# Kernel optimization log

Measured on AMD Instinct MI355X. Metric: run time of the kernel, lower is better.

Reference implementation:

```python
import jax, jax.numpy as jnp
import numpy as np

N = 100000   # nodes
E = 1600000  # edges
G = 64       # graphs in batch
DIMS = [(7, 128), (128, 128), (128, 256)]
EPS = 1e-5


def setup_inputs() -> dict:
    key = jax.random.key(0)
    ks = jax.random.split(key, 32)
    inp = {}
    inp["x"] = jax.random.normal(ks[0], (N, 7), dtype=jnp.float32)
    inp["edge_index"] = jax.random.randint(ks[1], (2, E), 0, N, dtype=jnp.int64)
    inp["batch"] = jnp.sort(jax.random.randint(ks[2], (N,), 0, G, dtype=jnp.int64))
    ki = 3
    for i, (din, dout) in enumerate(DIMS):
        inp[f"Wl{i}"] = jax.random.normal(ks[ki], (din, dout), dtype=jnp.float32) * 0.05; ki += 1
        inp[f"bl{i}"] = jnp.zeros((dout,), dtype=jnp.float32)
        inp[f"Wr{i}"] = jax.random.normal(ks[ki], (din, dout), dtype=jnp.float32) * 0.05; ki += 1
        inp[f"g{i}"] = jax.random.uniform(ks[ki], (dout,), dtype=jnp.float32) + 0.5; ki += 1
        inp[f"be{i}"] = jax.random.normal(ks[ki], (dout,), dtype=jnp.float32) * 0.1; ki += 1
        inp[f"rm{i}"] = jax.random.normal(ks[ki], (dout,), dtype=jnp.float32) * 0.1; ki += 1
        inp[f"rv{i}"] = jax.random.uniform(ks[ki], (dout,), dtype=jnp.float32) + 0.5; ki += 1
    return inp


def _sage(x, src, dst, Wl, bl, Wr):
    # mean-aggregate neighbor features: out[i] = mean_{(j->i)} x[j]
    agg = jax.ops.segment_sum(x[src], dst, num_segments=N)          # [N, din]
    cnt = jax.ops.segment_sum(jnp.ones((src.shape[0],), x.dtype), dst, num_segments=N)
    mean = agg / jnp.maximum(cnt, 1.0)[:, None]
    return x @ Wl + bl + mean @ Wr


def _bn_relu(x, g, be, rm, rv):
    # BatchNorm1d in eval mode (running stats) + ReLU; dropout is a no-op in eval
    return jax.nn.relu((x - rm) * jax.lax.rsqrt(rv + EPS) * g + be)


def reference(x, edge_index, batch,
              Wl0, bl0, Wr0, g0, be0, rm0, rv0,
              Wl1, bl1, Wr1, g1, be1, rm1, rv1,
              Wl2, bl2, Wr2, g2, be2, rm2, rv2):
    src, dst = edge_index[0], edge_index[1]
    layers = [(Wl0, bl0, Wr0, g0, be0, rm0, rv0),
              (Wl1, bl1, Wr1, g1, be1, rm1, rv1),
              (Wl2, bl2, Wr2, g2, be2, rm2, rv2)]
    for Wl, bl, Wr, g, be, rm, rv in layers:
        x = _sage(x, src, dst, Wl, bl, Wr)
        x = _bn_relu(x, g, be, rm, rv)
    pooled = jax.ops.segment_sum(x, batch, num_segments=G)  # global_add_pool
    return (pooled, x)
```

## Files before the change

### kernel.cpp

```cpp
#include <hip/hip_runtime.h>
#include <hip/hip_bf16.h>

#define EPSV 1e-5f
#define PSHIFT 6
#define PMASK 63
#define PCAP 1536
#define B1SHIFT 11
#define B1MASK ((1 << B1SHIFT) - 1)
#define B1CAP 34816
#define SPLIT 16

typedef __attribute__((ext_vector_type(8))) short bf16x8;
typedef __attribute__((ext_vector_type(4))) float f32x4;
typedef __attribute__((ext_vector_type(4))) unsigned u32x4;

__device__ __forceinline__ float bf2f(unsigned short u) {
    unsigned x = ((unsigned)u) << 16;
    return __builtin_bit_cast(float, x);
}
__device__ __forceinline__ unsigned short f2bf(float f) {
    unsigned x = __builtin_bit_cast(unsigned, f);
    unsigned r = (x + 0x7fffu + ((x >> 16) & 1u)) >> 16;
    return (unsigned short)r;
}
__device__ __forceinline__ f32x4 bflo4(u32x4 v) {
    f32x4 r;
    r.x = __builtin_bit_cast(float, v.x << 16);
    r.y = __builtin_bit_cast(float, v.y << 16);
    r.z = __builtin_bit_cast(float, v.z << 16);
    r.w = __builtin_bit_cast(float, v.w << 16);
    return r;
}
__device__ __forceinline__ f32x4 bfhi4(u32x4 v) {
    f32x4 r;
    r.x = __builtin_bit_cast(float, v.x & 0xffff0000u);
    r.y = __builtin_bit_cast(float, v.y & 0xffff0000u);
    r.z = __builtin_bit_cast(float, v.z & 0xffff0000u);
    r.w = __builtin_bit_cast(float, v.w & 0xffff0000u);
    return r;
}


__global__ __launch_bounds__(256) void k_scatter1(const int* __restrict__ src,
                                                  const int* __restrict__ dst,
                                                  int* __restrict__ bcnt1,
                                                  unsigned* __restrict__ stg1,
                                                  int E, int NB1) {
    __shared__ int hist[64], sbase[64], scur[64];
    int t = threadIdx.x;
    int base = blockIdx.x * 2048;
    if (t < 64) { hist[t] = 0; scur[t] = 0; }
    __syncthreads();
    unsigned val[8];
    int cb[8];
#pragma unroll
    for (int k = 0; k < 8; k++) {
        int i = base + k * 256 + t;
        if (i < E) {
            int d = __builtin_nontemporal_load(&dst[i]);
            int s = __builtin_nontemporal_load(&src[i]);
            cb[k] = d >> B1SHIFT;
            val[k] = ((unsigned)s << B1SHIFT) | (unsigned)(d & B1MASK);
            atomicAdd(&hist[cb[k]], 1);
        } else
            cb[k] = -1;
    }
    __syncthreads();
    if (t < NB1 && hist[t] > 0) sbase[t] = atomicAdd(&bcnt1[t], hist[t]);
    __syncthreads();
#pragma unroll
    for (int k = 0; k < 8; k++) {
        if (cb[k] >= 0) {
            int r = atomicAdd(&scur[cb[k]], 1);
            int slot = sbase[cb[k]] + r;
            if (slot < B1CAP) stg1[(size_t)cb[k] * B1CAP + slot] = val[k];
        }
    }
}

__global__ __launch_bounds__(256) void k_scatter2(const int* __restrict__ bcnt1,
                                                  const unsigned* __restrict__ stg1,
                                                  int* __restrict__ pcnt,
                                                  unsigned* __restrict__ pstg) {
    __shared__ int hist[32], sbase[32], scur[32];
    int cb = blockIdx.x >> 4;
    int sl = blockIdx.x & (SPLIT - 1);
    int t = threadIdx.x;
    if (t < 32) { hist[t] = 0; scur[t] = 0; }
    int cnt = min(bcnt1[cb], B1CAP);
    int per = (cnt + SPLIT - 1) / SPLIT;
    int lo = sl * per, hi = min(lo + per, cnt);
    __syncthreads();
    const unsigned* sp = stg1 + (size_t)cb * B1CAP;
    for (int j = lo + t; j < hi; j += 256)
        atomicAdd(&hist[(sp[j] >> 6) & 31], 1);
    __syncthreads();
    if (t < 32 && hist[t] > 0) sbase[t] = atomicAdd(&pcnt[(cb << 5) + t], hist[t]);
    __syncthreads();
    for (int j = lo + t; j < hi; j += 256) {
        unsigned v = sp[j];
        int pr = (v >> 6) & 31;
        int r = atomicAdd(&scur[pr], 1);
        int slot = sbase[pr] + r;
        if (slot < PCAP)
            pstg[(size_t)((cb << 5) + pr) * PCAP + slot] =
                ((v >> 5) & ~63u) | (v & 63u);
    }
}

__global__ __launch_bounds__(256) void k_meta(const int* __restrict__ pcnt,
                                              int* __restrict__ pbase,
                                              int* __restrict__ off,
                                              const int* __restrict__ batch,
                                              int* __restrict__ gstart,
                                              int NPART, int Nn, int G) {
    if (blockIdx.x == 1) {
        int g = threadIdx.x;
        if (g > G) return;
        if (g == G) {
            gstart[G] = Nn;
            return;
        }
        int lo = 0, hi = Nn;
        while (lo < hi) {
            int mid = (lo + hi) >> 1;
            if (batch[mid] < g) lo = mid + 1;
            else hi = mid;
        }
        gstart[g] = lo;
        return;
    }
    __shared__ int red[256];
    int t = threadIdx.x;
    int chunk = (NPART + 255) / 256;
    int lo = t * chunk, hi = min(lo + chunk, NPART);
    int s = 0;
    for (int p = lo; p < hi; p++) {
        int tt = min(pcnt[p], PCAP);
        pbase[p] = tt;
        s += tt;
    }
    red[t] = s;
    __syncthreads();
    for (int d = 1; d < 256; d <<= 1) {
        int v = (t >= d) ? red[t - d] : 0;
        __syncthreads();
        red[t] += v;
        __syncthreads();
    }
    int base = (t == 0) ? 0 : red[t - 1];
    for (int p = lo; p < hi; p++) {
        int tt = pbase[p];
        pbase[p] = base;
        base += tt;
    }
    if (t == 255) off[Nn] = red[255];
}

__global__ __launch_bounds__(256) void k_build(const int* __restrict__ pcnt,
                                               const unsigned* __restrict__ pstg,
                                               const int* __restrict__ pbase,
                                               int* __restrict__ off,
                                               int* __restrict__ csr, int Nn) {
    __shared__ unsigned ed[PCAP];
    __shared__ int srt[PCAP];
    __shared__ int cnt[64], loff[64], cur[64];
    int p = blockIdx.x, t = threadIdx.x;
    int tot = min(pcnt[p], PCAP);
    if (t < 64) cnt[t] = 0;
    __syncthreads();
    const unsigned* sp = pstg + (size_t)p * PCAP;
    for (int j = t; j < tot; j += 256) {
        unsigned e = __builtin_nontemporal_load(&sp[j]);
        ed[j] = e;
        atomicAdd(&cnt[e & PMASK], 1);
    }
    __syncthreads();
    if (t == 0) {
        int a = 0;
        for (int j = 0; j < 64; j++) {
            loff[j] = a;
            cur[j] = a;
            a += cnt[j];
        }
    }
    __syncthreads();
    int base = pbase[p];
    int node0 = p << PSHIFT;
    if (t < 64 && node0 + t < Nn) off[node0 + t] = base + loff[t];
    for (int j = t; j < tot; j += 256) {
        unsigned e = ed[j];
        int pos = atomicAdd(&cur[e & PMASK], 1);
        srt[pos] = (int)(e >> PSHIFT);
    }
    __syncthreads();
    for (int j = t; j < tot; j += 256) csr[base + j] = srt[j];
}


__global__ __launch_bounds__(256) void k_agg7(const float* __restrict__ x,
                                              const int* __restrict__ off,
                                              const int* __restrict__ csr,
                                              float* __restrict__ mean, int n) {
    int i = (blockIdx.x * 256 + threadIdx.x) >> 3;
    int r = threadIdx.x & 7;
    if (i >= n) return;
    int a = off[i], b = off[i + 1];
    float acc = 0.f;
    if (r < 7) {
        int j = a;
        for (; j + 1 < b; j += 2)
            acc += x[(size_t)csr[j] * 7 + r] + x[(size_t)csr[j + 1] * 7 + r];
        if (j < b) acc += x[(size_t)csr[j] * 7 + r];
    }
    float inv = 1.0f / (float)max(b - a, 1);
    if (r < 7) mean[(size_t)i * 7 + r] = acc * inv;
}

__global__ __launch_bounds__(256) void k_agg128(const unsigned short* __restrict__ x,
                                                const int* __restrict__ off,
                                                const int* __restrict__ csr,
                                                unsigned short* __restrict__ mean,
                                                int n) {
    int q = (blockIdx.x * 256 + threadIdx.x) >> 4;
    int sl = threadIdx.x & 15;
    if (q >= n) return;
    int a = off[q], b = off[q + 1];
    const u32x4* xr = (const u32x4*)x;
    f32x4 aL = {0.f, 0.f, 0.f, 0.f}, aH = {0.f, 0.f, 0.f, 0.f};
    int j = a;
    for (; j + 3 < b; j += 4) {
        int s0 = csr[j], s1 = csr[j + 1], s2 = csr[j + 2], s3 = csr[j + 3];
        u32x4 v0 = xr[(size_t)s0 * 16 + sl];
        u32x4 v1 = xr[(size_t)s1 * 16 + sl];
        u32x4 v2 = xr[(size_t)s2 * 16 + sl];
        u32x4 v3 = xr[(size_t)s3 * 16 + sl];
        aL += bflo4(v0) + bflo4(v1) + bflo4(v2) + bflo4(v3);
        aH += bfhi4(v0) + bfhi4(v1) + bfhi4(v2) + bfhi4(v3);
    }
    for (; j < b; j++) {
        u32x4 v = xr[(size_t)csr[j] * 16 + sl];
        aL += bflo4(v);
        aH += bfhi4(v);
    }
    float inv = 1.0f / (float)max(b - a, 1);
    u32x4 o;
    o.x = (unsigned)f2bf(aL.x * inv) | ((unsigned)f2bf(aH.x * inv) << 16);
    o.y = (unsigned)f2bf(aL.y * inv) | ((unsigned)f2bf(aH.y * inv) << 16);
    o.z = (unsigned)f2bf(aL.z * inv) | ((unsigned)f2bf(aH.z * inv) << 16);
    o.w = (unsigned)f2bf(aL.w * inv) | ((unsigned)f2bf(aH.w * inv) << 16);
    __builtin_nontemporal_store(o, (u32x4*)mean + (size_t)q * 16 + sl);
}


__global__ __launch_bounds__(256) void k_prepw_all(
    const float* __restrict__ Wl1, const float* __restrict__ Wr1,
    const float* __restrict__ Wl2, const float* __restrict__ Wr2,
    unsigned short* __restrict__ Wlt1, unsigned short* __restrict__ Wrt1,
    unsigned short* __restrict__ Wlt2, unsigned short* __restrict__ Wrt2) {
    int u = blockIdx.x * 256 + threadIdx.x;
    const float* W;
    unsigned short* Wt;
    int Ncols, v;
    if (u < 32768) {
        v = u & 16383;
        W = (u < 16384) ? Wl1 : Wr1;
        Wt = (u < 16384) ? Wlt1 : Wrt1;
        Ncols = 128;
    } else {
        v = (u - 32768) & 32767;
        W = (u < 65536) ? Wl2 : Wr2;
        Wt = (u < 65536) ? Wlt2 : Wrt2;
        Ncols = 256;
    }
    int n = v % Ncols, k = v / Ncols;
    Wt[(size_t)n * 128 + k] = f2bf(W[(size_t)k * Ncols + n]);
}


__global__ __launch_bounds__(256) void k_layer0(
    const float* __restrict__ x, const float* __restrict__ mean,
    const float* __restrict__ Wl, const float* __restrict__ bl,
    const float* __restrict__ Wr, const float* __restrict__ g,
    const float* __restrict__ be, const float* __restrict__ rm,
    const float* __restrict__ rv, unsigned short* __restrict__ out, int n) {
    int tid = threadIdx.x;
    int col = tid & 127;
    int r = tid >> 7;
    int row = blockIdx.x * 2 + r;
    if (row >= n) return;
    float sc = g[col] * rsqrtf(rv[col] + EPSV);
    float sh = (bl[col] - rm[col]) * sc + be[col];
    const float* xp = x + (size_t)row * 7;
    const float* mp = mean + (size_t)row * 7;
    float acc = 0.f;
#pragma unroll
    for (int k = 0; k < 7; k++) acc += xp[k] * Wl[k * 128 + col];
#pragma unroll
    for (int k = 0; k < 7; k++) acc += mp[k] * Wr[k * 128 + col];
    float h = acc * sc + sh;
    out[(size_t)row * 128 + col] = f2bf(fmaxf(h, 0.f));
}


template <int COLS, int DOUT, bool BF16OUT>
__global__ __launch_bounds__(256) void k_mfma_layer(
    const unsigned short* __restrict__ xin, const unsigned short* __restrict__ meanb,
    const unsigned short* __restrict__ Wlt, const unsigned short* __restrict__ Wrt,
    const float* __restrict__ bl, const float* __restrict__ g,
    const float* __restrict__ be, const float* __restrict__ rm,
    const float* __restrict__ rv, void* __restrict__ outv,
    const int* __restrict__ batchp, float* __restrict__ pooled, int n) {
    __shared__ unsigned short As[64 * 40];
    __shared__ unsigned short Bs[COLS * 40];
    __shared__ float plds[COLS];

    int tid = threadIdx.x;
    int wave = tid >> 6;
    int lane = tid & 63;
    int m = lane & 15;
    int half = lane >> 4;
    int row0 = blockIdx.x * 64;
    int colbase = blockIdx.y * COLS;

    if (!BF16OUT && tid < COLS) plds[tid] = 0.f;

    const int NCB = COLS / 16;
    f32x4 acc[NCB] = {};

    for (int s = 0; s < 8; s++) {
        int pass = s >> 2;
        int k0 = (s & 3) * 32;
        const unsigned short* Asrc = pass ? meanb : xin;
        const unsigned short* Wt = pass ? Wrt : Wlt;

        __syncthreads();
        {
            int rr = tid >> 2;
            int ks = (tid & 3) * 8;
            int grow = row0 + rr;
            float4 v = make_float4(0.f, 0.f, 0.f, 0.f);
            if (grow < n) v = *(const float4*)&Asrc[(size_t)grow * 128 + k0 + ks];
            *(float4*)&As[rr * 40 + ks] = v;
        }
#pragma unroll
        for (int rep = 0; rep < COLS / 64; rep++) {
            int u = tid + rep * 256;
            int nn = u >> 2;
            int ks = (u & 3) * 8;
            float4 v = *(const float4*)&Wt[(size_t)(colbase + nn) * 128 + k0 + ks];
            *(float4*)&Bs[nn * 40 + ks] = v;
        }
        __syncthreads();

        bf16x8 a = *(const bf16x8*)&As[(wave * 16 + m) * 40 + half * 8];
#pragma unroll
        for (int cb = 0; cb < NCB; cb++) {
            bf16x8 b = *(const bf16x8*)&Bs[(cb * 16 + m) * 40 + half * 8];
            acc[cb] = __builtin_amdgcn_mfma_f32_16x16x32_bf16(a, b, acc[cb], 0, 0, 0);
        }
    }

    bool uni = true;
    int gmin = 0;
    if (!BF16OUT) {
        int last = min(row0 + 63, n - 1);
        gmin = batchp[row0];
        uni = (gmin == batchp[last]);
    }

    float* outf = (float*)outv;
    unsigned short* outb = (unsigned short*)outv;
    float colsum[NCB];
#pragma unroll
    for (int cb = 0; cb < NCB; cb++) colsum[cb] = 0.f;

#pragma unroll
    for (int cb = 0; cb < NCB; cb++) {
        int col = colbase + cb * 16 + m;
        float sc = g[col] * rsqrtf(rv[col] + EPSV);
        float sh = (bl[col] - rm[col]) * sc + be[col];
#pragma unroll
        for (int reg = 0; reg < 4; reg++) {
            int r0 = row0 + wave * 16 + half * 4 + reg;
            if (r0 < n) {
                float h = fmaxf(acc[cb][reg] * sc + sh, 0.f);
                if (BF16OUT) {
                    outb[(size_t)r0 * DOUT + col] = f2bf(h);
                } else {
                    outf[(size_t)r0 * DOUT + col] = h;
                    if (uni) colsum[cb] += h;
                    else atomicAdd(&pooled[(size_t)batchp[r0] * 256 + col], h);
                }
            }
        }
    }

    if (!BF16OUT) {
        if (uni) {
#pragma unroll
            for (int cb = 0; cb < NCB; cb++) atomicAdd(&plds[cb * 16 + m], colsum[cb]);
            __syncthreads();
            if (tid < COLS)
                atomicAdd(&pooled[(size_t)gmin * 256 + colbase + tid], plds[tid]);
        }
    }
}


extern "C" void kernel_launch(void* const* d_in, const int* in_sizes, int n_in,
                              void* d_out, int out_size, void* d_ws, size_t ws_size,
                              hipStream_t stream) {
    const float* x = (const float*)d_in[0];
    const int* ei = (const int*)d_in[1];
    const int* batch = (const int*)d_in[2];
    const int N = in_sizes[0] / 7;
    const int E = in_sizes[1] / 2;
    const int G = 64;
    const int* src = ei;
    const int* dst = ei + E;
    const int NPART = (N + PMASK) >> PSHIFT;
    const int NB1 = (N + (1 << B1SHIFT) - 1) >> B1SHIFT;

    const float* P[21];
    for (int i = 0; i < 21; i++) P[i] = (const float*)d_in[3 + i];
    const float **L0 = P, **L1 = P + 7, **L2 = P + 14;

    char* w = (char*)d_ws;
    auto carve = [&](size_t bytes) {
        void* p = (void*)w;
        w += (bytes + 255) & ~(size_t)255;
        return p;
    };
    int* cnts = (int*)carve((size_t)(64 + NPART) * 4);
    int* bcnt1 = cnts;
    int* pcnt = cnts + 64;
    unsigned* stg1 = (unsigned*)carve((size_t)NB1 * B1CAP * 4);
    unsigned* pstg = (unsigned*)carve((size_t)NPART * PCAP * 4);
    int* pbase = (int*)carve((size_t)NPART * 4);
    int* off = (int*)carve(((size_t)N + 1) * 4);
    int* gstart = (int*)carve(((size_t)G + 1) * 4);
    float* mean7 = (float*)carve((size_t)N * 7 * 4);
    unsigned short* x1 = (unsigned short*)carve((size_t)N * 128 * 2);
    unsigned short* meanb = (unsigned short*)carve((size_t)N * 128 * 2);
    unsigned short* Wlt1 = (unsigned short*)carve((size_t)128 * 128 * 2);
    unsigned short* Wrt1 = (unsigned short*)carve((size_t)128 * 128 * 2);
    unsigned short* Wlt2 = (unsigned short*)carve((size_t)128 * 256 * 2);
    unsigned short* Wrt2 = (unsigned short*)carve((size_t)128 * 256 * 2);
    int* csr = (int*)stg1;

    float* pooled = (float*)d_out;
    float* x3 = (float*)d_out + (size_t)G * 256;

    hipMemsetAsync(cnts, 0, (size_t)(64 + NPART) * 4, stream);
    hipMemsetAsync(pooled, 0, (size_t)G * 256 * 4, stream);

    k_scatter1<<<(E + 2047) / 2048, 256, 0, stream>>>(src, dst, bcnt1, stg1, E, NB1);
    k_scatter2<<<NB1 * SPLIT, 256, 0, stream>>>(bcnt1, stg1, pcnt, pstg);
    k_meta<<<2, 256, 0, stream>>>(pcnt, pbase, off, batch, gstart, NPART, N, G);
    k_build<<<NPART, 256, 0, stream>>>(pcnt, pstg, pbase, off, csr, N);
    k_prepw_all<<<(98304 + 255) / 256, 256, 0, stream>>>(L1[0], L1[2], L2[0], L2[2],
                                                         Wlt1, Wrt1, Wlt2, Wrt2);

    k_agg7<<<(N * 8 + 255) / 256, 256, 0, stream>>>(x, off, csr, mean7, N);
    k_layer0<<<(N + 1) / 2, 256, 0, stream>>>(x, mean7, L0[0], L0[1], L0[2], L0[3],
                                              L0[4], L0[5], L0[6], x1, N);

    k_agg128<<<((size_t)N * 16 + 255) / 256, 256, 0, stream>>>(x1, off, csr, meanb, N);
    k_mfma_layer<128, 128, true><<<dim3((N + 63) / 64, 1), 256, 0, stream>>>(
        x1, meanb, Wlt1, Wrt1, L1[1], L1[3], L1[4], L1[5], L1[6], x1, nullptr,
        nullptr, N);

    k_agg128<<<((size_t)N * 16 + 255) / 256, 256, 0, stream>>>(x1, off, csr, meanb, N);
    k_mfma_layer<128, 256, false><<<dim3((N + 63) / 64, 2), 256, 0, stream>>>(
        x1, meanb, Wlt2, Wrt2, L2[1], L2[3], L2[4], L2[5], L2[6], x3, batch,
        pooled, N);
}
```

Baseline: 510.6 us.

## Prefetch MFMA tiles into registers, deepen agg unroll, pool two-graph blocks locally

The aggregation kernel now gathers 8 neighbors per iteration and reads the CSR index stream with nontemporal loads. The mean output switches to a normal store so the following layer can hit it in cache. The MFMA layer kernel prefetches the next K-slice of A and B tiles into registers while the current slice is computed, overlapping global loads with LDS staging and MFMA. The pooling epilogue also handles blocks that span two consecutive graphs with LDS reductions, avoiding per-element global atomics for those blocks. This costs more registers and a second LDS reduction buffer.

```diff
diff --git a/kernel.cpp b/kernel.cpp
--- a/kernel.cpp
+++ b/kernel.cpp
@@ -229,17 +229,35 @@
     const u32x4* xr = (const u32x4*)x;
     f32x4 aL = {0.f, 0.f, 0.f, 0.f}, aH = {0.f, 0.f, 0.f, 0.f};
     int j = a;
+    for (; j + 7 < b; j += 8) {
+        u32x4 v[8];
+#pragma unroll
+        for (int t = 0; t < 8; t++) {
+            int s = __builtin_nontemporal_load(&csr[j + t]);
+            v[t] = xr[(size_t)s * 16 + sl];
+        }
+#pragma unroll
+        for (int t = 0; t < 8; t++) {
+            aL += bflo4(v[t]);
+            aH += bfhi4(v[t]);
+        }
+    }
     for (; j + 3 < b; j += 4) {
-        int s0 = csr[j], s1 = csr[j + 1], s2 = csr[j + 2], s3 = csr[j + 3];
-        u32x4 v0 = xr[(size_t)s0 * 16 + sl];
-        u32x4 v1 = xr[(size_t)s1 * 16 + sl];
-        u32x4 v2 = xr[(size_t)s2 * 16 + sl];
-        u32x4 v3 = xr[(size_t)s3 * 16 + sl];
-        aL += bflo4(v0) + bflo4(v1) + bflo4(v2) + bflo4(v3);
-        aH += bfhi4(v0) + bfhi4(v1) + bfhi4(v2) + bfhi4(v3);
+        u32x4 v[4];
+#pragma unroll
+        for (int t = 0; t < 4; t++) {
+            int s = __builtin_nontemporal_load(&csr[j + t]);
+            v[t] = xr[(size_t)s * 16 + sl];
+        }
+#pragma unroll
+        for (int t = 0; t < 4; t++) {
+            aL += bflo4(v[t]);
+            aH += bfhi4(v[t]);
+        }
     }
     for (; j < b; j++) {
-        u32x4 v = xr[(size_t)csr[j] * 16 + sl];
+        int s = __builtin_nontemporal_load(&csr[j]);
+        u32x4 v = xr[(size_t)s * 16 + sl];
         aL += bflo4(v);
         aH += bfhi4(v);
     }
@@ -249,7 +267,7 @@
     o.y = (unsigned)f2bf(aL.y * inv) | ((unsigned)f2bf(aH.y * inv) << 16);
     o.z = (unsigned)f2bf(aL.z * inv) | ((unsigned)f2bf(aH.z * inv) << 16);
     o.w = (unsigned)f2bf(aL.w * inv) | ((unsigned)f2bf(aH.w * inv) << 16);
-    __builtin_nontemporal_store(o, (u32x4*)mean + (size_t)q * 16 + sl);
+    *((u32x4*)mean + (size_t)q * 16 + sl) = o;
 }
 
 
@@ -310,10 +328,11 @@
     const float* __restrict__ bl, const float* __restrict__ g,
     const float* __restrict__ be, const float* __restrict__ rm,
     const float* __restrict__ rv, void* __restrict__ outv,
-    const int* __restrict__ batchp, float* __restrict__ pooled, int n) {
+    const int* __restrict__ batchp, const int* __restrict__ gstartp,
+    float* __restrict__ pooled, int n) {
     __shared__ unsigned short As[64 * 40];
     __shared__ unsigned short Bs[COLS * 40];
-    __shared__ float plds[COLS];
+    __shared__ float plds[2 * COLS];
 
     int tid = threadIdx.x;
     int wave = tid >> 6;
@@ -323,34 +342,40 @@
     int row0 = blockIdx.x * 64;
     int colbase = blockIdx.y * COLS;
 
-    if (!BF16OUT && tid < COLS) plds[tid] = 0.f;
+    if (!BF16OUT) {
+        for (int u = tid; u < 2 * COLS; u += 256) plds[u] = 0.f;
+    }
 
     const int NCB = COLS / 16;
+    const int NREP = COLS / 64;
     f32x4 acc[NCB] = {};
 
-    for (int s = 0; s < 8; s++) {
+    int rr = tid >> 2;
+    int ks = (tid & 3) * 8;
+
+    float4 ra;
+    float4 rb[NREP];
+    auto issue = [&](int s) {
         int pass = s >> 2;
         int k0 = (s & 3) * 32;
         const unsigned short* Asrc = pass ? meanb : xin;
         const unsigned short* Wt = pass ? Wrt : Wlt;
-
+        int grow = row0 + rr;
+        ra = make_float4(0.f, 0.f, 0.f, 0.f);
+        if (grow < n) ra = *(const float4*)&Asrc[(size_t)grow * 128 + k0 + ks];
+#pragma unroll
+        for (int rep = 0; rep < NREP; rep++)
+            rb[rep] = *(const float4*)&Wt[(size_t)(colbase + rr + rep * 64) * 128 + k0 + ks];
+    };
+
+    issue(0);
+    for (int s = 0; s < 8; s++) {
         __syncthreads();
-        {
-            int rr = tid >> 2;
-            int ks = (tid & 3) * 8;
-            int grow = row0 + rr;
-            float4 v = make_float4(0.f, 0.f, 0.f, 0.f);
-            if (grow < n) v = *(const float4*)&Asrc[(size_t)grow * 128 + k0 + ks];
-            *(float4*)&As[rr * 40 + ks] = v;
-        }
-#pragma unroll
-        for (int rep = 0; rep < COLS / 64; rep++) {
-            int u = tid + rep * 256;
-            int nn = u >> 2;
-            int ks = (u & 3) * 8;
-            float4 v = *(const float4*)&Wt[(size_t)(colbase + nn) * 128 + k0 + ks];
-            *(float4*)&Bs[nn * 40 + ks] = v;
-        }
+        *(float4*)&As[rr * 40 + ks] = ra;
+#pragma unroll
+        for (int rep = 0; rep < NREP; rep++)
+            *(float4*)&Bs[(rr + rep * 64) * 40 + ks] = rb[rep];
+        if (s < 7) issue(s + 1);
         __syncthreads();
 
         bf16x8 a = *(const bf16x8*)&As[(wave * 16 + m) * 40 + half * 8];
@@ -361,19 +386,21 @@
         }
     }
 
-    bool uni = true;
-    int gmin = 0;
+    int gA = 0, gB = 0, gsplit = 0x7fffffff;
+    bool fast = true;
     if (!BF16OUT) {
         int last = min(row0 + 63, n - 1);
-        gmin = batchp[row0];
-        uni = (gmin == batchp[last]);
+        gA = batchp[row0];
+        gB = batchp[last];
+        if (gB == gA + 1) gsplit = gstartp[gB];
+        else if (gB != gA) fast = false;
     }
 
     float* outf = (float*)outv;
     unsigned short* outb = (unsigned short*)outv;
-    float colsum[NCB];
-#pragma unroll
-    for (int cb = 0; cb < NCB; cb++) colsum[cb] = 0.f;
+    float csA[NCB], csB[NCB];
+#pragma unroll
+    for (int cb = 0; cb < NCB; cb++) { csA[cb] = 0.f; csB[cb] = 0.f; }
 
 #pragma unroll
     for (int cb = 0; cb < NCB; cb++) {
@@ -389,20 +416,30 @@
                     outb[(size_t)r0 * DOUT + col] = f2bf(h);
                 } else {
                     outf[(size_t)r0 * DOUT + col] = h;
-                    if (uni) colsum[cb] += h;
-                    else atomicAdd(&pooled[(size_t)batchp[r0] * 256 + col], h);
+                    if (fast) {
+                        if (r0 < gsplit) csA[cb] += h;
+                        else csB[cb] += h;
+                    } else {
+                        atomicAdd(&pooled[(size_t)batchp[r0] * 256 + col], h);
+                    }
                 }
             }
         }
     }
 
-    if (!BF16OUT) {
-        if (uni) {
-#pragma unroll
-            for (int cb = 0; cb < NCB; cb++) atomicAdd(&plds[cb * 16 + m], colsum[cb]);
-            __syncthreads();
-            if (tid < COLS)
-                atomicAdd(&pooled[(size_t)gmin * 256 + colbase + tid], plds[tid]);
+    if (!BF16OUT && fast) {
+        bool two = (gsplit != 0x7fffffff);
+#pragma unroll
+        for (int cb = 0; cb < NCB; cb++) {
+            atomicAdd(&plds[cb * 16 + m], csA[cb]);
+            if (two) atomicAdd(&plds[COLS + cb * 16 + m], csB[cb]);
+        }
+        __syncthreads();
+        for (int u = tid; u < 2 * COLS; u += 256) {
+            int rsel = (u >= COLS);
+            if (rsel && !two) continue;
+            int c = u - rsel * COLS;
+            atomicAdd(&pooled[(size_t)(rsel ? gB : gA) * 256 + colbase + c], plds[u]);
         }
     }
 }
@@ -469,10 +506,10 @@
     k_agg128<<<((size_t)N * 16 + 255) / 256, 256, 0, stream>>>(x1, off, csr, meanb, N);
     k_mfma_layer<128, 128, true><<<dim3((N + 63) / 64, 1), 256, 0, stream>>>(
         x1, meanb, Wlt1, Wrt1, L1[1], L1[3], L1[4], L1[5], L1[6], x1, nullptr,
-        nullptr, N);
+        nullptr, nullptr, N);
 
     k_agg128<<<((size_t)N * 16 + 255) / 256, 256, 0, stream>>>(x1, off, csr, meanb, N);
     k_mfma_layer<128, 256, false><<<dim3((N + 63) / 64, 2), 256, 0, stream>>>(
         x1, meanb, Wlt2, Wrt2, L2[1], L2[3], L2[4], L2[5], L2[6], x3, batch,
-        pooled, N);
-}
+        gstart, pooled, N);
+}
```

New measurement: 550.2 us. +7.8%, slower.

## Replace per-block pooled atomics with two-graph partial sums and a reduction kernel

Applied to the files above, without the earlier changes.

The final layer now splits each 64-row block's column sums into at most two graph segments, using gstart to find the boundary, and writes them to a workspace instead of issuing global atomics. A new k_poolred kernel then reduces these per-block partials per graph. The aim is to cut global atomic contention on the pooled output and the per-element fallback atomics for blocks that straddle a graph boundary. The cost is an extra launch and extra workspace traffic. The mean store in the aggregation kernel is also changed from a nontemporal store to a normal store, so the following layer may hit in cache.

```diff
diff --git a/kernel.cpp b/kernel.cpp
--- a/kernel.cpp
+++ b/kernel.cpp
@@ -249,7 +249,7 @@
     o.y = (unsigned)f2bf(aL.y * inv) | ((unsigned)f2bf(aH.y * inv) << 16);
     o.z = (unsigned)f2bf(aL.z * inv) | ((unsigned)f2bf(aH.z * inv) << 16);
     o.w = (unsigned)f2bf(aL.w * inv) | ((unsigned)f2bf(aH.w * inv) << 16);
-    __builtin_nontemporal_store(o, (u32x4*)mean + (size_t)q * 16 + sl);
+    *((u32x4*)mean + (size_t)q * 16 + sl) = o;
 }
 
 
@@ -310,10 +310,12 @@
     const float* __restrict__ bl, const float* __restrict__ g,
     const float* __restrict__ be, const float* __restrict__ rm,
     const float* __restrict__ rv, void* __restrict__ outv,
-    const int* __restrict__ batchp, float* __restrict__ pooled, int n) {
+    const int* __restrict__ batchp, const int* __restrict__ gstartp,
+    int* __restrict__ wsgid, float* __restrict__ wspool,
+    float* __restrict__ pooled, int n) {
     __shared__ unsigned short As[64 * 40];
     __shared__ unsigned short Bs[COLS * 40];
-    __shared__ float plds[COLS];
+    __shared__ float plds[2 * COLS];
 
     int tid = threadIdx.x;
     int wave = tid >> 6;
@@ -323,7 +325,8 @@
     int row0 = blockIdx.x * 64;
     int colbase = blockIdx.y * COLS;
 
-    if (!BF16OUT && tid < COLS) plds[tid] = 0.f;
+    if (!BF16OUT)
+        for (int u = tid; u < 2 * COLS; u += 256) plds[u] = 0.f;
 
     const int NCB = COLS / 16;
     f32x4 acc[NCB] = {};
@@ -361,19 +364,21 @@
         }
     }
 
-    bool uni = true;
-    int gmin = 0;
+    int gA = 0, gB = 0, gsplit = 0x7fffffff;
+    bool fast = true;
     if (!BF16OUT) {
         int last = min(row0 + 63, n - 1);
-        gmin = batchp[row0];
-        uni = (gmin == batchp[last]);
+        gA = batchp[row0];
+        gB = batchp[last];
+        if (gB == gA + 1) gsplit = gstartp[gB];
+        else if (gB != gA) fast = false;
     }
 
     float* outf = (float*)outv;
     unsigned short* outb = (unsigned short*)outv;
-    float colsum[NCB];
-#pragma unroll
-    for (int cb = 0; cb < NCB; cb++) colsum[cb] = 0.f;
+    float csA[NCB], csB[NCB];
+#pragma unroll
+    for (int cb = 0; cb < NCB; cb++) { csA[cb] = 0.f; csB[cb] = 0.f; }
 
 #pragma unroll
     for (int cb = 0; cb < NCB; cb++) {
@@ -389,22 +394,55 @@
                     outb[(size_t)r0 * DOUT + col] = f2bf(h);
                 } else {
                     outf[(size_t)r0 * DOUT + col] = h;
-                    if (uni) colsum[cb] += h;
-                    else atomicAdd(&pooled[(size_t)batchp[r0] * 256 + col], h);
+                    if (fast) {
+                        if (r0 < gsplit) csA[cb] += h;
+                        else csB[cb] += h;
+                    } else {
+                        atomicAdd(&pooled[(size_t)batchp[r0] * 256 + col], h);
+                    }
                 }
             }
         }
     }
 
     if (!BF16OUT) {
-        if (uni) {
-#pragma unroll
-            for (int cb = 0; cb < NCB; cb++) atomicAdd(&plds[cb * 16 + m], colsum[cb]);
-            __syncthreads();
-            if (tid < COLS)
-                atomicAdd(&pooled[(size_t)gmin * 256 + colbase + tid], plds[tid]);
-        }
-    }
+        bool two = (gsplit != 0x7fffffff);
+        if (fast) {
+#pragma unroll
+            for (int cb = 0; cb < NCB; cb++) {
+                atomicAdd(&plds[cb * 16 + m], csA[cb]);
+                if (two) atomicAdd(&plds[COLS + cb * 16 + m], csB[cb]);
+            }
+        }
+        __syncthreads();
+        size_t bx = blockIdx.x;
+        for (int u = tid; u < COLS; u += 256) {
+            wspool[(bx * 2 + 0) * DOUT + colbase + u] = plds[u];
+            wspool[(bx * 2 + 1) * DOUT + colbase + u] = plds[COLS + u];
+        }
+        if (tid < 2)
+            wsgid[bx * 2 + tid] =
+                !fast ? -1 : (tid == 0 ? gA : (two ? gB : -1));
+    }
+}
+
+
+__global__ __launch_bounds__(256) void k_poolred(const float* __restrict__ wspool,
+                                                 const int* __restrict__ wsgid,
+                                                 const int* __restrict__ gstart,
+                                                 float* __restrict__ pooled) {
+    int g = blockIdx.x;
+    int col = threadIdx.x;
+    int r0 = gstart[g], r1 = gstart[g + 1];
+    if (r1 <= r0) return;
+    int b0 = r0 >> 6, b1 = (r1 - 1) >> 6;
+    float acc = 0.f;
+    for (int bx = b0; bx <= b1; bx++) {
+        int ga = wsgid[bx * 2], gb = wsgid[bx * 2 + 1];
+        if (ga == g) acc += wspool[((size_t)bx * 2 + 0) * 256 + col];
+        if (gb == g) acc += wspool[((size_t)bx * 2 + 1) * 256 + col];
+    }
+    atomicAdd(&pooled[(size_t)g * 256 + col], acc);
 }
 
 
@@ -421,6 +459,7 @@
     const int* dst = ei + E;
     const int NPART = (N + PMASK) >> PSHIFT;
     const int NB1 = (N + (1 << B1SHIFT) - 1) >> B1SHIFT;
+    const int NBX = (N + 63) / 64;
 
     const float* P[21];
     for (int i = 0; i < 21; i++) P[i] = (const float*)d_in[3 + i];
@@ -447,6 +486,8 @@
     unsigned short* Wrt1 = (unsigned short*)carve((size_t)128 * 128 * 2);
     unsigned short* Wlt2 = (unsigned short*)carve((size_t)128 * 256 * 2);
     unsigned short* Wrt2 = (unsigned short*)carve((size_t)128 * 256 * 2);
+    float* wspool = (float*)carve((size_t)NBX * 2 * 256 * 4);
+    int* wsgid = (int*)carve((size_t)NBX * 2 * 4);
     int* csr = (int*)stg1;
 
     float* pooled = (float*)d_out;
@@ -467,12 +508,14 @@
                                               L0[4], L0[5], L0[6], x1, N);
 
     k_agg128<<<((size_t)N * 16 + 255) / 256, 256, 0, stream>>>(x1, off, csr, meanb, N);
-    k_mfma_layer<128, 128, true><<<dim3((N + 63) / 64, 1), 256, 0, stream>>>(
-        x1, meanb, Wlt1, Wrt1, L1[1], L1[3], L1[4], L1[5], L1[6], x1, nullptr,
-        nullptr, N);
+    k_mfma_layer<128, 128, true><<<dim3(NBX, 1), 256, 0, stream>>>(
+        x1, meanb, Wlt1, Wrt1, L1[1], L1[3], L1[4], L1[5], L1[6], x1,
+        nullptr, nullptr, nullptr, nullptr, nullptr, N);
 
     k_agg128<<<((size_t)N * 16 + 255) / 256, 256, 0, stream>>>(x1, off, csr, meanb, N);
-    k_mfma_layer<128, 256, false><<<dim3((N + 63) / 64, 2), 256, 0, stream>>>(
-        x1, meanb, Wlt2, Wrt2, L2[1], L2[3], L2[4], L2[5], L2[6], x3, batch,
-        pooled, N);
-}
+    k_mfma_layer<128, 256, false><<<dim3(NBX, 2), 256, 0, stream>>>(
+        x1, meanb, Wlt2, Wrt2, L2[1], L2[3], L2[4], L2[5], L2[6], x3,
+        batch, gstart, wsgid, wspool, pooled, N);
+
+    k_poolred<<<G, 256, 0, stream>>>(wspool, wsgid, gstart, pooled);
+}
```

After: 496.3 us. 1.03x faster.
